# Kernel tuning notes

Measured on AMD Instinct MI355X. Metric: run time of the kernel, lower is better.

## Reference

```python
import jax, jax.numpy as jnp
import numpy as np

L, B, T, V, E, H = 6, 4, 1024, 32000, 768, 12
D = E // H  # head_size = 64


def setup_inputs() -> dict:
    key = jax.random.key(0)
    ks = jax.random.split(key, 12)
    s = 0.02
    n = lambda k, shape: jax.random.normal(k, shape, jnp.float32) * s
    return {
        "idx": jax.random.randint(ks[0], (B, T), 0, V),
        "tok_emb": n(ks[1], (V, E)),
        "pos_emb": n(ks[2], (T, E)),
        "ln1_w": jnp.ones((L, E)), "ln1_b": jnp.zeros((L, E)),
        "wq": n(ks[3], (L, E, H, D)),
        "wk": n(ks[4], (L, E, H, D)),
        "wv": n(ks[5], (L, E, H, D)),
        "wo": n(ks[6], (L, E, E)), "bo": jnp.zeros((L, E)),
        "ln2_w": jnp.ones((L, E)), "ln2_b": jnp.zeros((L, E)),
        "w1": n(ks[7], (L, E, 4 * E)), "b1": jnp.zeros((L, 4 * E)),
        "w2": n(ks[8], (L, 4 * E, E)), "b2": jnp.zeros((L, E)),
        "lnf_w": jnp.ones((E,)), "lnf_b": jnp.zeros((E,)),
        "head_w": n(ks[9], (E, V)), "head_b": jnp.zeros((V,)),
    }


def _ln(x, w, b, eps=1e-5):
    m = x.mean(-1, keepdims=True)
    v = ((x - m) ** 2).mean(-1, keepdims=True)
    return (x - m) * jax.lax.rsqrt(v + eps) * w + b


def _forward(idx, tok_emb, pos_emb, ln1_w, ln1_b, wq, wk, wv, wo, bo,
             ln2_w, ln2_b, w1, b1, w2, b2, lnf_w, lnf_b, head_w, head_b):
    t = idx.shape[1]
    x = tok_emb[idx] + pos_emb[None, :t]          # [B,T,E]
    causal = jnp.tril(jnp.ones((t, t), bool))     # tril buffer
    scale = jnp.asarray(D, x.dtype) ** -0.5       # k.shape[-1] ** -0.5

    def block(x, p):
        l1w, l1b, Wq, Wk, Wv, Wo, Bo, l2w, l2b, W1, B1, W2, B2 = p
        h = _ln(x, l1w, l1b)
        q = jnp.einsum('btc,chd->bthd', h, Wq)
        k = jnp.einsum('btc,chd->bthd', h, Wk)
        v = jnp.einsum('btc,chd->bthd', h, Wv)
        wei = jnp.einsum('bqhd,bkhd->bhqk', q, k) * scale
        wei = jnp.where(causal, wei, -jnp.inf)
        wei = jax.nn.softmax(wei, axis=-1)
        att = jnp.einsum('bhqk,bkhd->bqhd', wei, v).reshape(x.shape)
        x = x + (att @ Wo + Bo)
        h2 = _ln(x, l2w, l2b)
        x = x + (jax.nn.relu(h2 @ W1 + B1) @ W2 + B2)
        return x, None

    params = (ln1_w, ln1_b, wq, wk, wv, wo, bo, ln2_w, ln2_b, w1, b1, w2, b2)
    x, _ = jax.lax.scan(block, x, params)
    x = _ln(x, lnf_w, lnf_b)
    return x @ head_w + head_b                    # [B,T,V] logits


def reference(idx, tok_emb, pos_emb, ln1_w, ln1_b, wq, wk, wv, wo, bo,
              ln2_w, ln2_b, w1, b1, w2, b2, lnf_w, lnf_b, head_w, head_b):
    return _forward(idx, tok_emb, pos_emb, ln1_w, ln1_b, wq, wk, wv, wo, bo,
                    ln2_w, ln2_b, w1, b1, w2, b2, lnf_w, lnf_b, head_w, head_b)
```

## Files before the change

### kernel.cpp

```cpp
#include <hip/hip_runtime.h>
#include <hip/hip_bf16.h>
#include <math.h>

#define L_LAYERS 6
#define BB 4
#define TT 1024
#define VV 32000
#define EE 768
#define HH 12
#define DD 64
#define BT (BB * TT)

typedef unsigned short u16;
typedef unsigned int   u32;
typedef __attribute__((ext_vector_type(8))) short short8;
typedef __attribute__((ext_vector_type(8))) unsigned short ushort8v;
typedef __attribute__((ext_vector_type(4))) unsigned short ushort4v;
typedef __attribute__((ext_vector_type(4))) float f32x4;

__device__ __forceinline__ float b2f_lo(u32 u) { union { u32 i; float f; } c; c.i = u << 16;          return c.f; }
__device__ __forceinline__ float b2f_hi(u32 u) { union { u32 i; float f; } c; c.i = u & 0xffff0000u;  return c.f; }
__device__ __forceinline__ u16  f2b(float f)   { union { float f; u32 i; } c{f}; u32 r = c.i + 0x7fffu + ((c.i >> 16) & 1u); return (u16)(r >> 16); }

__device__ __forceinline__ void gload16(const void* g, void* l) {
    __builtin_amdgcn_global_load_lds(
        (const __attribute__((address_space(1))) void*)g,
        (__attribute__((address_space(3))) void*)l, 16, 0, 0);
}

#define WT_LAYER 7077888u
#define WT_HEAD_OFF ((size_t)L_LAYERS * WT_LAYER)

__global__ __launch_bounds__(256) void embed_kernel(
    const int* __restrict__ idx, const float* __restrict__ tok_emb,
    const float* __restrict__ pos_emb, float* __restrict__ x)
{
    int i = blockIdx.x * 256 + threadIdx.x;
    int e  = i % EE;
    int bt = i / EE;
    int t  = bt % TT;
    int tok = idx[bt];
    x[i] = tok_emb[(size_t)tok * EE + e] + pos_emb[(size_t)t * EE + e];
}

__global__ __launch_bounds__(256) void ln_kernel(
    const float* __restrict__ X, const float* __restrict__ w,
    const float* __restrict__ b, u16* __restrict__ Y)
{
    const int lane = threadIdx.x & 63;
    const size_t row = blockIdx.x * 4 + (threadIdx.x >> 6);
    const float* x = X + row * EE;

    f32x4 v[3];
    #pragma unroll
    for (int k = 0; k < 3; k++)
        v[k] = *(const f32x4*)&x[lane * 4 + k * 256];

    float s = 0.0f;
    #pragma unroll
    for (int k = 0; k < 3; k++) s += v[k][0] + v[k][1] + v[k][2] + v[k][3];
    #pragma unroll
    for (int off = 32; off; off >>= 1) s += __shfl_xor(s, off);
    const float mean = s * (1.0f / EE);

    float q = 0.0f;
    #pragma unroll
    for (int k = 0; k < 3; k++)
        #pragma unroll
        for (int j = 0; j < 4; j++) {
            v[k][j] -= mean;
            q += v[k][j] * v[k][j];
        }
    #pragma unroll
    for (int off = 32; off; off >>= 1) q += __shfl_xor(q, off);
    const float rstd = rsqrtf(q * (1.0f / EE) + 1e-5f);

    u16* y = Y + row * EE;
    #pragma unroll
    for (int k = 0; k < 3; k++) {
        const f32x4 wv = *(const f32x4*)&w[lane * 4 + k * 256];
        const f32x4 bv = *(const f32x4*)&b[lane * 4 + k * 256];
        ushort4v o;
        #pragma unroll
        for (int j = 0; j < 4; j++) o[j] = f2b(v[k][j] * rstd * wv[j] + bv[j]);
        *(ushort4v*)&y[lane * 4 + k * 256] = o;
    }
}

__device__ __forceinline__ void transpose_tile(
    const float* __restrict__ W, u16* __restrict__ Wt,
    int K, int N, int kt, int nt)
{
    __shared__ float t[32][33];
    const int k0 = kt * 32;
    const int n0 = nt * 32;
    const int c = threadIdx.x & 31;
    const int r = threadIdx.x >> 5;
    #pragma unroll
    for (int i = 0; i < 4; i++)
        t[r + i * 8][c] = W[(size_t)(k0 + r + i * 8) * N + n0 + c];
    __syncthreads();
    #pragma unroll
    for (int i = 0; i < 4; i++) {
        int rr = r + i * 8;
        Wt[(size_t)(n0 + rr) * K + k0 + c] = f2b(t[c][rr]);
    }
}

__device__ __forceinline__ void transpose_layer_core(
    const float* wq, const float* wk, const float* wv, const float* wo,
    const float* w1, const float* w2, u16* wt, int t)
{
    if (t < 2304) {
        const int m = t / 576, r = t % 576;
        const float* Ws[4] = {wq, wk, wv, wo};
        transpose_tile(Ws[m], wt + (size_t)m * 768 * 768, 768, 768, r / 24, r % 24);
    } else if (t < 4608) {
        const int r = t - 2304;
        transpose_tile(w1, wt + (size_t)4 * 768 * 768, 768, 3072, r / 96, r % 96);
    } else {
        const int r = t - 4608;
        transpose_tile(w2, wt + (size_t)4 * 768 * 768 + (size_t)3072 * 768,
                       3072, 768, r / 24, r % 24);
    }
}

__global__ __launch_bounds__(256) void transpose_layer(
    const float* __restrict__ wq, const float* __restrict__ wk,
    const float* __restrict__ wv, const float* __restrict__ wo,
    const float* __restrict__ w1, const float* __restrict__ w2,
    u16* __restrict__ wt)
{
    transpose_layer_core(wq, wk, wv, wo, w1, w2, wt, blockIdx.x);
}

__global__ __launch_bounds__(256) void transpose_cvt(
    const float* __restrict__ W, u16* __restrict__ Wt, int K, int N)
{
    transpose_tile(W, Wt, K, N, blockIdx.y, blockIdx.x);
}

__global__ __launch_bounds__(256) void transpose_all(
    const float* __restrict__ wq, const float* __restrict__ wk,
    const float* __restrict__ wv, const float* __restrict__ wo,
    const float* __restrict__ w1, const float* __restrict__ w2,
    const float* __restrict__ head_w, u16* __restrict__ wt)
{
    const int t = blockIdx.x;
    if (t < L_LAYERS * 6912) {
        const int l = t / 6912, r = t % 6912;
        const size_t oEE = (size_t)l * EE * EE;
        const size_t oEF = (size_t)l * EE * 4 * EE;
        transpose_layer_core(wq + oEE, wk + oEE, wv + oEE, wo + oEE,
                             w1 + oEF, w2 + oEF,
                             wt + (size_t)l * WT_LAYER, r);
    } else {
        const int r = t - L_LAYERS * 6912;
        transpose_tile(head_w, wt + WT_HEAD_OFF, 768, 32000, r / 1000, r % 1000);
    }
}

template<int RELU, int RES, int OUTBF, int MFRAG>
__global__ __launch_bounds__(256) void gemm_bf16(
    const u16* __restrict__ A, const u16* __restrict__ Bt,
    const float* __restrict__ bias, const float* __restrict__ res,
    void* __restrict__ Cv, int M, int N, int K)
{
    constexpr int TM = MFRAG * 32;
    __shared__ u16 As[TM * 64];
    __shared__ u16 Bs[128 * 64];

    const int tid  = threadIdx.x;
    const int lane = tid & 63;
    const int w    = tid >> 6;
    const int wr   = w >> 1, wc = w & 1;
    const int m0 = blockIdx.x * TM;
    const int n0 = blockIdx.y * 128;

    const int cs = (lane & 7) ^ (lane >> 3);
    const int rl = lane >> 3;

    int aoff[2 * MFRAG], boff[8];
    const int kq = lane >> 4;
    #pragma unroll
    for (int mi = 0; mi < MFRAG; mi++) {
        int rg = wr * (MFRAG * 16) + mi * 16 + (lane & 15);
        #pragma unroll
        for (int ks = 0; ks < 2; ks++)
            aoff[2 * mi + ks] = rg * 64 + (((ks * 4 + kq) ^ (rg & 7)) * 8);
    }
    #pragma unroll
    for (int ni = 0; ni < 4; ni++) {
        int rg = wc * 64 + ni * 16 + (lane & 15);
        #pragma unroll
        for (int ks = 0; ks < 2; ks++)
            boff[2 * ni + ks] = rg * 64 + (((ks * 4 + kq) ^ (rg & 7)) * 8);
    }

    f32x4 acc[MFRAG][4] = {};

    for (int k0 = 0; k0 < K; k0 += 64) {
        __syncthreads();
        #pragma unroll
        for (int i = 0; i < MFRAG; i++) {
            const int seg = i * 4 + w;
            const int row = seg * 8 + rl;
            gload16(A + (size_t)(m0 + row) * K + k0 + cs * 8, &As[seg * 512]);
        }
        #pragma unroll
        for (int i = 0; i < 4; i++) {
            const int seg = i * 4 + w;
            const int row = seg * 8 + rl;
            gload16(Bt + (size_t)(n0 + row) * K + k0 + cs * 8, &Bs[seg * 512]);
        }
        __syncthreads();
        #pragma unroll
        for (int ks = 0; ks < 2; ks++) {
            short8 af[MFRAG], bfv[4];
            #pragma unroll
            for (int mi = 0; mi < MFRAG; mi++) af[mi] = *(const short8*)&As[aoff[2 * mi + ks]];
            #pragma unroll
            for (int ni = 0; ni < 4; ni++) bfv[ni] = *(const short8*)&Bs[boff[2 * ni + ks]];
            #pragma unroll
            for (int mi = 0; mi < MFRAG; mi++)
                #pragma unroll
                for (int ni = 0; ni < 4; ni++)
                    acc[mi][ni] = __builtin_amdgcn_mfma_f32_16x16x32_bf16(
                        af[mi], bfv[ni], acc[mi][ni], 0, 0, 0);
        }
    }

    const int rbase = m0 + wr * (MFRAG * 16) + (lane >> 4) * 4;
    const int cbase = n0 + wc * 64 + (lane & 15);
    #pragma unroll
    for (int ni = 0; ni < 4; ni++) {
        const int c = cbase + ni * 16;
        const float bv = bias ? bias[c] : 0.0f;
        #pragma unroll
        for (int mi = 0; mi < MFRAG; mi++) {
            const int r = rbase + mi * 16;
            #pragma unroll
            for (int i = 0; i < 4; i++) {
                float v = acc[mi][ni][i] + bv;
                const size_t off = (size_t)(r + i) * N + c;
                if (RES)  v += res[off];
                if (RELU) v = fmaxf(v, 0.0f);
                if (OUTBF) {
                    ((u16*)Cv)[off] = f2b(v);
                } else if (!RES) {
                    __builtin_nontemporal_store(v, &((float*)Cv)[off]);
                } else {
                    ((float*)Cv)[off] = v;
                }
            }
        }
    }
}

#define AST 72
__global__ __launch_bounds__(256) void attn_mfma(
    const u16* __restrict__ qkv, u16* __restrict__ O)
{
    const int tid = threadIdx.x;
    const int qi = blockIdx.x;
    const int h  = blockIdx.y;
    const int b  = blockIdx.z;
    const int q0 = qi * 64;

    __shared__ u16 Ks[2][64 * 64];
    __shared__ u16 Vt[2][80 * AST];
    __shared__ u16 Ps[64 * AST];

    const int lane = tid & 63;
    const int w    = tid >> 6;
    const int lr   = lane & 15;
    const int lk   = lane >> 4;

    const int cs = (lane & 7) ^ (lane >> 3);
    const int rl = lane >> 3;
    const int vk2 = tid & 31;
    const int vdc = tid >> 5;

    for (int i = tid; i < 16 * AST; i += 256) {
        const int r = i / AST, c = i % AST;
        const u16 v = (r == 0) ? (u16)0x3F80 : (u16)0;
        Vt[0][(64 + r) * AST + c] = v;
        Vt[1][(64 + r) * AST + c] = v;
    }

    {
        const int sr = tid >> 2, sc = tid & 3;
        const u16* src = qkv + (size_t)(b * TT + q0 + sr) * 2304 + h * 64 + sc * 16;
        *(ushort8v*)&Ps[sr * AST + sc * 16]     = *(const ushort8v*)src;
        *(ushort8v*)&Ps[sr * AST + sc * 16 + 8] = *(const ushort8v*)(src + 8);
    }
    __syncthreads();
    short8 aq[2];
    #pragma unroll
    for (int ks = 0; ks < 2; ks++)
        aq[ks] = *(const short8*)&Ps[(w * 16 + lr) * AST + lk * 8 + ks * 32];

    ushort8v vr0, vr1;
    auto K_ISSUE = [&](int t, int bf) {
        const int k0 = t * 64;
        #pragma unroll
        for (int j = 0; j < 2; ++j) {
            const int seg = j * 4 + w;
            const int row = seg * 8 + rl;
            gload16(qkv + (size_t)(b * TT + k0 + row) * 2304 + 768 + h * 64 + cs * 8,
                    &Ks[bf][seg * 512]);
        }
    };
    auto V_LOAD = [&](int t) {
        const int k0 = t * 64;
        const u16* p = qkv + (size_t)(b * TT + k0 + 2 * vk2) * 2304 + 1536 + h * 64 + vdc * 8;
        vr0 = *(const ushort8v*)p;
        vr1 = *(const ushort8v*)(p + 2304);
    };
    auto V_WRITE = [&](int bf) {
        #pragma unroll
        for (int j = 0; j < 8; ++j) {
            const u32 val = (u32)vr0[j] | ((u32)vr1[j] << 16);
            *(u32*)&Vt[bf][(vdc * 8 + j) * AST + 2 * vk2] = val;
        }
    };

    K_ISSUE(0, 0);
    V_LOAD(0);
    V_WRITE(0);
    __syncthreads();

    f32x4 oacc[5] = {};
    float m_run[4];
    #pragma unroll
    for (int i = 0; i < 4; i++) m_run[i] = -3.0e38f;

    const int qrow = q0 + w * 16 + lk * 4;
    const float SC = 0.18033688f;

    for (int t = 0; t <= qi; ++t) {
        const int cur = t & 1;

        f32x4 sfrag[4] = {};
        #pragma unroll
        for (int ks = 0; ks < 2; ks++)
            #pragma unroll
            for (int nt = 0; nt < 4; nt++) {
                const int rg = nt * 16 + lr;
                short8 bk = *(const short8*)&Ks[cur][rg * 64 + (((ks * 4 + lk) ^ (rg & 7)) * 8)];
                sfrag[nt] = __builtin_amdgcn_mfma_f32_16x16x32_bf16(aq[ks], bk, sfrag[nt], 0, 0, 0);
            }

        if (t < qi) { K_ISSUE(t + 1, cur ^ 1); V_LOAD(t + 1); }

        const int k0 = t * 64;
        float sv[4][4], mxv[4];
        float need = 0.0f;
        #pragma unroll
        for (int i = 0; i < 4; i++) {
            float mx = -3.0e38f;
            #pragma unroll
            for (int nt = 0; nt < 4; nt++) {
                float s = sfrag[nt][i] * SC;
                if (t == qi && (k0 + nt * 16 + lr) > (qrow + i)) s = -3.0e38f;
                sv[i][nt] = s;
                mx = fmaxf(mx, s);
            }
            mx = fmaxf(mx, __shfl_xor(mx, 1));
            mx = fmaxf(mx, __shfl_xor(mx, 2));
            mx = fmaxf(mx, __shfl_xor(mx, 4));
            mx = fmaxf(mx, __shfl_xor(mx, 8));
            mxv[i] = mx;
            need = fmaxf(need, mx - m_run[i]);
        }
        if (!__all(need <= 11.5f)) {
            #pragma unroll
            for (int i = 0; i < 4; i++) {
                const float m_new = fmaxf(m_run[i], mxv[i]);
                const float scale = exp2f(m_run[i] - m_new);
                #pragma unroll
                for (int dt = 0; dt < 5; dt++) oacc[dt][i] *= scale;
                m_run[i] = m_new;
            }
        }
        #pragma unroll
        for (int i = 0; i < 4; i++)
            #pragma unroll
            for (int nt = 0; nt < 4; nt++)
                sv[i][nt] = exp2f(sv[i][nt] - m_run[i]);

        #pragma unroll
        for (int i = 0; i < 4; i++)
            #pragma unroll
            for (int nt = 0; nt < 4; nt++)
                Ps[(w * 16 + lk * 4 + i) * AST + nt * 16 + lr] = f2b(sv[i][nt]);

        #pragma unroll
        for (int ks = 0; ks < 2; ks++) {
            short8 ap = *(const short8*)&Ps[(w * 16 + lr) * AST + lk * 8 + ks * 32];
            #pragma unroll
            for (int dt = 0; dt < 5; dt++) {
                short8 bv = *(const short8*)&Vt[cur][(dt * 16 + lr) * AST + lk * 8 + ks * 32];
                oacc[dt] = __builtin_amdgcn_mfma_f32_16x16x32_bf16(ap, bv, oacc[dt], 0, 0, 0);
            }
        }

        if (t < qi) V_WRITE(cur ^ 1);
        __syncthreads();
    }

    #pragma unroll
    for (int i = 0; i < 4; i++) {
        const float li  = __shfl(oacc[4][i], lane & 48);
        const float inv = 1.0f / li;
        u16* dst = O + (size_t)(b * TT + q0 + w * 16 + lk * 4 + i) * 768 + h * 64 + lr;
        #pragma unroll
        for (int dt = 0; dt < 4; dt++)
            dst[dt * 16] = f2b(oacc[dt][i] * inv);
    }
}

extern "C" void kernel_launch(void* const* d_in, const int* in_sizes, int n_in,
                              void* d_out, int out_size, void* d_ws, size_t ws_size,
                              hipStream_t stream)
{
    (void)in_sizes; (void)n_in; (void)out_size;

    const int*   idx     = (const int*)  d_in[0];
    const float* tok_emb = (const float*)d_in[1];
    const float* pos_emb = (const float*)d_in[2];
    const float* ln1_w   = (const float*)d_in[3];
    const float* ln1_b   = (const float*)d_in[4];
    const float* wq      = (const float*)d_in[5];
    const float* wk      = (const float*)d_in[6];
    const float* wv      = (const float*)d_in[7];
    const float* wo      = (const float*)d_in[8];
    const float* bo      = (const float*)d_in[9];
    const float* ln2_w   = (const float*)d_in[10];
    const float* ln2_b   = (const float*)d_in[11];
    const float* w1      = (const float*)d_in[12];
    const float* b1      = (const float*)d_in[13];
    const float* w2      = (const float*)d_in[14];
    const float* b2      = (const float*)d_in[15];
    const float* lnf_w   = (const float*)d_in[16];
    const float* lnf_b   = (const float*)d_in[17];
    const float* head_w  = (const float*)d_in[18];
    const float* head_b  = (const float*)d_in[19];
    float* out = (float*)d_out;

    const size_t S = (size_t)BT * EE;
    float* x   = (float*)d_ws;
    u16*  qkv  = (u16*)(x + S);
    u16*  hb   = qkv + (size_t)BT * 2304;
    u16*  ffh  = hb + S;
    u16*  wt   = ffh + (size_t)BT * 3072;

    const size_t need_big = 62914560u + 134086656u + 1024;
    const bool big = (ws_size >= need_big);

    embed_kernel<<<BT * EE / 256, 256, 0, stream>>>(idx, tok_emb, pos_emb, x);

    if (big)
        transpose_all<<<L_LAYERS * 6912 + 24000, 256, 0, stream>>>(
            wq, wk, wv, wo, w1, w2, head_w, wt);

    for (int l = 0; l < L_LAYERS; l++) {
        const size_t oE  = (size_t)l * EE;
        const size_t oEE = (size_t)l * EE * EE;
        const size_t oEF = (size_t)l * EE * 4 * EE;
        u16* wtl = big ? (wt + (size_t)l * WT_LAYER) : wt;

        if (!big)
            transpose_layer<<<6912, 256, 0, stream>>>(
                wq + oEE, wk + oEE, wv + oEE, wo + oEE, w1 + oEF, w2 + oEF, wtl);

        ln_kernel<<<BT / 4, 256, 0, stream>>>(x, ln1_w + oE, ln1_b + oE, hb);
        gemm_bf16<0, 0, 1, 4><<<dim3(BT / 128, 2304 / 128), 256, 0, stream>>>(
            hb, wtl, nullptr, nullptr, qkv, BT, 2304, 768);
        attn_mfma<<<dim3(TT / 64, HH, BB), 256, 0, stream>>>(qkv, hb);
        gemm_bf16<0, 1, 0, 2><<<dim3(BT / 64, 768 / 128), 256, 0, stream>>>(
            hb, wtl + (size_t)3 * 768 * 768, bo + oE, x, x, BT, 768, 768);
        ln_kernel<<<BT / 4, 256, 0, stream>>>(x, ln2_w + oE, ln2_b + oE, hb);
        gemm_bf16<1, 0, 1, 4><<<dim3(BT / 128, 3072 / 128), 256, 0, stream>>>(
            hb, wtl + (size_t)4 * 768 * 768, b1 + (size_t)l * 4 * EE, nullptr, ffh, BT, 3072, 768);
        gemm_bf16<0, 1, 0, 2><<<dim3(BT / 64, 768 / 128), 256, 0, stream>>>(
            ffh, wtl + (size_t)4 * 768 * 768 + (size_t)3072 * 768, b2 + oE, x, x, BT, 768, 3072);
    }

    ln_kernel<<<BT / 4, 256, 0, stream>>>(x, lnf_w, lnf_b, hb);
    u16* wth = big ? (wt + WT_HEAD_OFF) : wt;
    if (!big)
        transpose_cvt<<<dim3(VV / 32, EE / 32), 256, 0, stream>>>(head_w, wth, EE, VV);
    gemm_bf16<0, 0, 0, 4><<<dim3(BT / 128, VV / 128), 256, 0, stream>>>(
        hb, wth, head_b, nullptr, out, BT, VV, 768);
}
```

Before: 1.416 ms.

## Transpose QK^T MFMA so softmax runs per-row in-lane, drop ones-column row-sum trick

The QK^T MFMA operands are swapped so each lane holds one query row across keys. The row max now needs only two cross-lane shuffles, and the row sum is accumulated explicitly in a running l_run. The extra fifth V tile of ones, previously used to get row sums out of the PV MFMA, is removed, which cuts one MFMA per k-step and some LDS. P is written to LDS with packed 32-bit stores. The GEMM epilogue also drops the nontemporal store for non-residual fp32 outputs, which may change cache behaviour for large outputs such as the logits.

```diff
diff --git a/kernel.cpp b/kernel.cpp
--- a/kernel.cpp
+++ b/kernel.cpp
@@ -245,13 +245,8 @@
                 const size_t off = (size_t)(r + i) * N + c;
                 if (RES)  v += res[off];
                 if (RELU) v = fmaxf(v, 0.0f);
-                if (OUTBF) {
-                    ((u16*)Cv)[off] = f2b(v);
-                } else if (!RES) {
-                    __builtin_nontemporal_store(v, &((float*)Cv)[off]);
-                } else {
-                    ((float*)Cv)[off] = v;
-                }
+                if (OUTBF) ((u16*)Cv)[off] = f2b(v);
+                else       ((float*)Cv)[off] = v;
             }
         }
     }
@@ -268,7 +263,7 @@
     const int q0 = qi * 64;
 
     __shared__ u16 Ks[2][64 * 64];
-    __shared__ u16 Vt[2][80 * AST];
+    __shared__ u16 Vt[2][64 * AST];
     __shared__ u16 Ps[64 * AST];
 
     const int lane = tid & 63;
@@ -280,13 +275,6 @@
     const int rl = lane >> 3;
     const int vk2 = tid & 31;
     const int vdc = tid >> 5;
-
-    for (int i = tid; i < 16 * AST; i += 256) {
-        const int r = i / AST, c = i % AST;
-        const u16 v = (r == 0) ? (u16)0x3F80 : (u16)0;
-        Vt[0][(64 + r) * AST + c] = v;
-        Vt[1][(64 + r) * AST + c] = v;
-    }
 
     {
         const int sr = tid >> 2, sc = tid & 3;
@@ -330,12 +318,10 @@
     V_WRITE(0);
     __syncthreads();
 
-    f32x4 oacc[5] = {};
-    float m_run[4];
-    #pragma unroll
-    for (int i = 0; i < 4; i++) m_run[i] = -3.0e38f;
-
-    const int qrow = q0 + w * 16 + lk * 4;
+    f32x4 oacc[4] = {};
+    float m_run = -3.0e38f, l_run = 0.0f;
+
+    const int qrow = q0 + w * 16 + lr;
     const float SC = 0.18033688f;
 
     for (int t = 0; t <= qi; ++t) {
@@ -348,58 +334,68 @@
             for (int nt = 0; nt < 4; nt++) {
                 const int rg = nt * 16 + lr;
                 short8 bk = *(const short8*)&Ks[cur][rg * 64 + (((ks * 4 + lk) ^ (rg & 7)) * 8)];
-                sfrag[nt] = __builtin_amdgcn_mfma_f32_16x16x32_bf16(aq[ks], bk, sfrag[nt], 0, 0, 0);
+                sfrag[nt] = __builtin_amdgcn_mfma_f32_16x16x32_bf16(bk, aq[ks], sfrag[nt], 0, 0, 0);
             }
 
         if (t < qi) { K_ISSUE(t + 1, cur ^ 1); V_LOAD(t + 1); }
 
         const int k0 = t * 64;
-        float sv[4][4], mxv[4];
-        float need = 0.0f;
-        #pragma unroll
-        for (int i = 0; i < 4; i++) {
-            float mx = -3.0e38f;
-            #pragma unroll
-            for (int nt = 0; nt < 4; nt++) {
+        float sv[4][4];
+        float mx = -3.0e38f;
+        #pragma unroll
+        for (int nt = 0; nt < 4; nt++)
+            #pragma unroll
+            for (int i = 0; i < 4; i++) {
                 float s = sfrag[nt][i] * SC;
-                if (t == qi && (k0 + nt * 16 + lr) > (qrow + i)) s = -3.0e38f;
-                sv[i][nt] = s;
+                if (t == qi && (k0 + nt * 16 + lk * 4 + i) > qrow) s = -3.0e38f;
+                sv[nt][i] = s;
                 mx = fmaxf(mx, s);
             }
-            mx = fmaxf(mx, __shfl_xor(mx, 1));
-            mx = fmaxf(mx, __shfl_xor(mx, 2));
-            mx = fmaxf(mx, __shfl_xor(mx, 4));
-            mx = fmaxf(mx, __shfl_xor(mx, 8));
-            mxv[i] = mx;
-            need = fmaxf(need, mx - m_run[i]);
-        }
-        if (!__all(need <= 11.5f)) {
+        mx = fmaxf(mx, __shfl_xor(mx, 16));
+        mx = fmaxf(mx, __shfl_xor(mx, 32));
+
+        if (!__all(mx - m_run <= 11.5f)) {
+            const float m_new = fmaxf(m_run, mx);
+            const float scale = exp2f(m_run - m_new);
+            l_run *= scale;
+            float sc_i[4];
+            #pragma unroll
+            for (int i = 0; i < 4; i++)
+                sc_i[i] = __shfl(scale, (lane & 48) | (lk * 4 + i));
+            #pragma unroll
+            for (int dt = 0; dt < 4; dt++)
+                #pragma unroll
+                for (int i = 0; i < 4; i++) oacc[dt][i] *= sc_i[i];
+            m_run = m_new;
+        }
+
+        float rs = 0.0f;
+        #pragma unroll
+        for (int nt = 0; nt < 4; nt++)
             #pragma unroll
             for (int i = 0; i < 4; i++) {
-                const float m_new = fmaxf(m_run[i], mxv[i]);
-                const float scale = exp2f(m_run[i] - m_new);
-                #pragma unroll
-                for (int dt = 0; dt < 5; dt++) oacc[dt][i] *= scale;
-                m_run[i] = m_new;
+                const float p = exp2f(sv[nt][i] - m_run);
+                sv[nt][i] = p;
+                rs += p;
             }
-        }
-        #pragma unroll
-        for (int i = 0; i < 4; i++)
-            #pragma unroll
-            for (int nt = 0; nt < 4; nt++)
-                sv[i][nt] = exp2f(sv[i][nt] - m_run[i]);
-
-        #pragma unroll
-        for (int i = 0; i < 4; i++)
-            #pragma unroll
-            for (int nt = 0; nt < 4; nt++)
-                Ps[(w * 16 + lk * 4 + i) * AST + nt * 16 + lr] = f2b(sv[i][nt]);
+        rs += __shfl_xor(rs, 16);
+        rs += __shfl_xor(rs, 32);
+        l_run += rs;
+
+        #pragma unroll
+        for (int nt = 0; nt < 4; nt++) {
+            const u32 p0 = (u32)f2b(sv[nt][0]) | ((u32)f2b(sv[nt][1]) << 16);
+            const u32 p1 = (u32)f2b(sv[nt][2]) | ((u32)f2b(sv[nt][3]) << 16);
+            u16* dst = &Ps[(w * 16 + lr) * AST + nt * 16 + lk * 4];
+            *(u32*)dst       = p0;
+            *(u32*)(dst + 2) = p1;
+        }
 
         #pragma unroll
         for (int ks = 0; ks < 2; ks++) {
             short8 ap = *(const short8*)&Ps[(w * 16 + lr) * AST + lk * 8 + ks * 32];
             #pragma unroll
-            for (int dt = 0; dt < 5; dt++) {
+            for (int dt = 0; dt < 4; dt++) {
                 short8 bv = *(const short8*)&Vt[cur][(dt * 16 + lr) * AST + lk * 8 + ks * 32];
                 oacc[dt] = __builtin_amdgcn_mfma_f32_16x16x32_bf16(ap, bv, oacc[dt], 0, 0, 0);
             }
@@ -411,7 +407,7 @@
 
     #pragma unroll
     for (int i = 0; i < 4; i++) {
-        const float li  = __shfl(oacc[4][i], lane & 48);
+        const float li  = __shfl(l_run, (lane & 48) | (lk * 4 + i));
         const float inv = 1.0f / li;
         u16* dst = O + (size_t)(b * TT + q0 + w * 16 + lk * 4 + i) * 768 + h * 64 + lr;
         #pragma unroll
```

After: 1.479 ms. +4.5%, slower.
